# Kernel tuning notes

Hardware: AMD Instinct MI355X
Metric: run time of the kernel (lower is better)

## Reference

```python
import jax, jax.numpy as jnp
import numpy as np

TAU = 2.0
V_TH = 1.0
ALPHA = 2.0  # ATan surrogate alpha

@jax.custom_vjp
def spike_fn(x):
    return (x >= 0.0).astype(x.dtype)

def _spike_fwd(x):
    return spike_fn(x), x

def _spike_bwd(x, g):
    # spikingjelly ATan surrogate: alpha/2 / (1 + (pi/2*alpha*x)^2)
    return (g * (ALPHA / 2.0) / (1.0 + (jnp.pi / 2.0 * ALPHA * x) ** 2),)

spike_fn.defvjp(_spike_fwd, _spike_bwd)

def lif_step(v, h):
    # decay_input=True, v_reset=0: v += (h - v)/tau
    v = v + (h - v) / TAU
    s = spike_fn(v - V_TH)
    v = v * (1.0 - s)  # hard reset to v_reset=0
    return v, s

def setup_inputs() -> dict:
    key = jax.random.key(0)
    k1, k2, k3 = jax.random.split(key, 3)
    B, T, I, H, O = 128, 2048, 128, 1024, 128
    x = jax.random.normal(k1, (B, T, I), dtype=jnp.float32)
    W1 = jax.random.normal(k2, (H, I), dtype=jnp.float32) / np.sqrt(I)
    b1 = jnp.zeros((H,), dtype=jnp.float32)
    W2 = jax.random.normal(k3, (O, H), dtype=jnp.float32) / np.sqrt(H)
    b2 = jnp.zeros((O,), dtype=jnp.float32)
    return {"x": x, "W1": W1, "b1": b1, "W2": W2, "b2": b2}

def reference(x, W1, b1, W2, b2):
    B, T, I = x.shape
    H = W1.shape[0]
    O = W2.shape[0]
    xt = jnp.transpose(x, (1, 0, 2))  # [T, B, I]

    def step(carry, x_t):
        v1, v2 = carry
        h1 = x_t @ W1.T + b1
        v1, s1 = lif_step(v1, h1)
        h2 = s1 @ W2.T + b2
        v2, s2 = lif_step(v2, h2)
        return (v1, v2), s2

    v1_0 = jnp.zeros((B, H), dtype=x.dtype)
    v2_0 = jnp.zeros((B, O), dtype=x.dtype)
    _, outs = jax.lax.scan(step, (v1_0, v2_0), xt)  # [T, B, O]
    decision_start = T // 2
    return jnp.sum(outs[decision_start:], axis=0)  # [B, O]
```

## Files before the change

kernel.cpp:

```cpp
#include <hip/hip_runtime.h>
#include <stdint.h>

#define NB 128
#define NT 2048
#define NI 128
#define NH 1024
#define NO 128

typedef float f32x4 __attribute__((ext_vector_type(4)));
typedef float f32x16 __attribute__((ext_vector_type(16)));

__global__ __launch_bounds__(256) void w2p_kernel(
    const float* __restrict__ W2, float2* __restrict__ W2P)
{
    const int idx = blockIdx.x * 256 + threadIdx.x;
    const int k = idx >> 6;
    const int j = idx & 63;
    W2P[idx] = make_float2(W2[(size_t)j * NH + k], W2[(size_t)(j + 64) * NH + k]);
}

#define XL(DST, IMM)                                                      \
    asm volatile("s_load_dwordx16 %0, %1, " #IMM : "=s"(DST) : "s"(xb))

#define F16(ACC, XV)                                                      \
    do {                                                                  \
        ACC = fmaf(w0.x, (XV)[0],  ACC);                                  \
        ACC = fmaf(w0.y, (XV)[1],  ACC);                                  \
        ACC = fmaf(w0.z, (XV)[2],  ACC);                                  \
        ACC = fmaf(w0.w, (XV)[3],  ACC);                                  \
        ACC = fmaf(w1.x, (XV)[4],  ACC);                                  \
        ACC = fmaf(w1.y, (XV)[5],  ACC);                                  \
        ACC = fmaf(w1.z, (XV)[6],  ACC);                                  \
        ACC = fmaf(w1.w, (XV)[7],  ACC);                                  \
        ACC = fmaf(w2.x, (XV)[8],  ACC);                                  \
        ACC = fmaf(w2.y, (XV)[9],  ACC);                                  \
        ACC = fmaf(w2.z, (XV)[10], ACC);                                  \
        ACC = fmaf(w2.w, (XV)[11], ACC);                                  \
        ACC = fmaf(w3.x, (XV)[12], ACC);                                  \
        ACC = fmaf(w3.y, (XV)[13], ACC);                                  \
        ACC = fmaf(w3.z, (XV)[14], ACC);                                  \
        ACC = fmaf(w3.w, (XV)[15], ACC);                                  \
    } while (0)

#define KCHUNK(Q0, I0, I1, I2, I3)                                        \
    {                                                                     \
        f32x16 xv0, xv1, xv2, xv3;                                        \
        XL(xv0, I0); XL(xv1, I1); XL(xv2, I2); XL(xv3, I3);               \
        asm volatile("s_waitcnt lgkmcnt(0)"                               \
                     : "+s"(xv0), "+s"(xv1), "+s"(xv2), "+s"(xv3));       \
        const f32x4 w0 = wrow[(Q0) + 0];                                  \
        const f32x4 w1 = wrow[(Q0) + 1];                                  \
        const f32x4 w2 = wrow[(Q0) + 2];                                  \
        const f32x4 w3 = wrow[(Q0) + 3];                                  \
        F16(t0, xv0); F16(t1, xv1); F16(t2, xv2); F16(t3, xv3);           \
    }

#define LIFSTEP(TT, TACC)                                                 \
    {                                                                     \
        const float h1 = ((TACC + red[par][0][TT][lane]) +                \
                          (red[par][1][TT][lane] + red[par][2][TT][lane])) + \
                         bias;                                            \
        v = fmaf(h1 - v, 0.5f, v);                                        \
        const bool sp = (v >= 1.0f);                                      \
        v = sp ? 0.0f : v;                                                \
        const unsigned long long m = __ballot(sp);                        \
        if (lane == 0) s1w[(size_t)TT * NB * (NH / 64)] = (uint64_t)m;    \
    }

__global__ __launch_bounds__(256, 4) void snn_phaseA4(
    const float* __restrict__ x, const float* __restrict__ W1,
    const float* __restrict__ b1, uint64_t* __restrict__ s1bits)
{
    const int b = blockIdx.x >> 4;
    const int hg = blockIdx.x & 15;
    const int kq = __builtin_amdgcn_readfirstlane(threadIdx.x >> 6);
    const int lane = threadIdx.x & 63;
    const int h = hg * 64 + lane;

    __shared__ f32x4 wlds[64][33];
    __shared__ float red[2][3][4][64];

#pragma unroll
    for (int i = 0; i < 8; ++i) {
        const int c = threadIdx.x + i * 256;
        const int r = c >> 5;
        const int kc = c & 31;
        wlds[r][kc] = *reinterpret_cast<const f32x4*>(
            W1 + (size_t)(hg * 64 + r) * NI + kc * 4);
    }
    __syncthreads();

    const float bias = b1[h];
    const f32x4* __restrict__ wrow = &wlds[lane][0];
    const int wb = kq * 8;

    const float* xb = x + (size_t)b * NT * NI + kq * 32;
    uint64_t* s1w = s1bits + (size_t)b * (NH / 64) + hg;

    float v = 0.0f;
#pragma unroll 1
    for (int tc = 0; tc < NT; tc += 4) {
        float t0 = 0.f, t1 = 0.f, t2 = 0.f, t3 = 0.f;
        KCHUNK(wb + 0, 0x0,  0x200, 0x400, 0x600);
        KCHUNK(wb + 4, 0x40, 0x240, 0x440, 0x640);

        const int par = (tc >> 2) & 1;
        if (kq) {
            red[par][kq - 1][0][lane] = t0;
            red[par][kq - 1][1][lane] = t1;
            red[par][kq - 1][2][lane] = t2;
            red[par][kq - 1][3][lane] = t3;
        }
        __syncthreads();
        if (!kq) {
            LIFSTEP(0, t0);
            LIFSTEP(1, t1);
            LIFSTEP(2, t2);
            LIFSTEP(3, t3);
        }
        s1w += (size_t)4 * NB * (NH / 64);
        xb += 4 * NI;
    }
}

__global__ __launch_bounds__(256, 4) void snn_phaseB(
    const uint64_t* __restrict__ s1bits, const float2* __restrict__ W2P,
    float* __restrict__ h2)
{
    const int wv = threadIdx.x >> 6;
    const int lane = threadIdx.x & 63;
    const size_t m = (size_t)blockIdx.x * 4 + wv;

    const uint64_t* __restrict__ sb = s1bits + m * (NH / 64);
    float a0 = 0.f, a1 = 0.f;

#pragma unroll 1
    for (int wd = 0; wd < NH / 64; ++wd) {
        const uint64_t m64 = sb[wd];
        const uint32_t mlo = (uint32_t)__builtin_amdgcn_readfirstlane((int)(uint32_t)m64);
        const uint32_t mhi = (uint32_t)__builtin_amdgcn_readfirstlane((int)(uint32_t)(m64 >> 32));
        uint64_t msk = ((uint64_t)mhi << 32) | mlo;
        while (msk) {
            const int i = __builtin_ctzll(msk);
            msk &= (msk - 1);
            const size_t k = ((size_t)wd << 6) + i;
            const float2 ww = W2P[k * 64 + lane];
            a0 += ww.x;
            a1 += ww.y;
        }
    }
    h2[m * NO + lane] = a0;
    h2[m * NO + 64 + lane] = a1;
}

__global__ __launch_bounds__(64) void snn_phaseD(
    const float* __restrict__ h2, const float* __restrict__ b2,
    float* __restrict__ out)
{
    const int idx = blockIdx.x * 64 + threadIdx.x;
    const int b = idx >> 7;
    const int o = idx & 127;
    const float bias = b2[o];

    const float* __restrict__ p = h2 + (size_t)b * NO + o;
    float v = 0.f, c = 0.f;
#pragma unroll 16
    for (int t = 0; t < NT; ++t) {
        const float hh = p[(size_t)t * NB * NO] + bias;
        v = fmaf(hh - v, 0.5f, v);
        const bool s = (v >= 1.0f);
        v = s ? 0.f : v;
        if (t >= NT / 2) c += s ? 1.f : 0.f;
    }
    out[idx] = c;
}

extern "C" void kernel_launch(void* const* d_in, const int* in_sizes, int n_in,
                              void* d_out, int out_size, void* d_ws,
                              size_t ws_size, hipStream_t stream)
{
    const float* x  = (const float*)d_in[0];
    const float* W1 = (const float*)d_in[1];
    const float* b1 = (const float*)d_in[2];
    const float* W2 = (const float*)d_in[3];
    const float* b2 = (const float*)d_in[4];
    float* out = (float*)d_out;

    uint8_t* ws = (uint8_t*)d_ws;
    uint64_t* s1bits = (uint64_t*)ws;
    float2* W2P = (float2*)(ws + (size_t)NT * NB * (NH / 64) * 8);
    float* h2 = (float*)(ws + (size_t)NT * NB * (NH / 64) * 8 +
                         (size_t)NH * 64 * sizeof(float2));

    w2p_kernel<<<dim3((NH * 64) / 256), dim3(256), 0, stream>>>(W2, W2P);
    snn_phaseA4<<<dim3(NB * 16), dim3(256), 0, stream>>>(x, W1, b1, s1bits);
    snn_phaseB<<<dim3((NT * NB) / 4), dim3(256), 0, stream>>>(s1bits, W2P, h2);
    snn_phaseD<<<dim3(256), dim3(64), 0, stream>>>(h2, b2, out);
}
```

Baseline: 2.319 ms.

## Prefetch x tiles into LDS with async global_load_lds double buffering

Replaces the per-wave scalar s_load_dwordx16 fetches of x, which stalled on lgkmcnt(0) every chunk, with direct global-to-LDS async loads. Each step loads the next 4 timesteps of x into a double-buffered LDS tile while the current one is computed, and the FMAs read x from LDS as vectors. Occupancy hint drops from 4 to 3 blocks. This adds LDS traffic, a vmcnt wait before each barrier and lower occupancy in exchange for overlapping the x loads with compute.

```diff
diff --git a/kernel.cpp b/kernel.cpp
--- a/kernel.cpp
+++ b/kernel.cpp
@@ -8,7 +8,6 @@
 #define NO 128
 
 typedef float f32x4 __attribute__((ext_vector_type(4)));
-typedef float f32x16 __attribute__((ext_vector_type(16)));
 
 __global__ __launch_bounds__(256) void w2p_kernel(
     const float* __restrict__ W2, float2* __restrict__ W2P)
@@ -18,42 +17,6 @@
     const int j = idx & 63;
     W2P[idx] = make_float2(W2[(size_t)j * NH + k], W2[(size_t)(j + 64) * NH + k]);
 }
-
-#define XL(DST, IMM)                                                      \
-    asm volatile("s_load_dwordx16 %0, %1, " #IMM : "=s"(DST) : "s"(xb))
-
-#define F16(ACC, XV)                                                      \
-    do {                                                                  \
-        ACC = fmaf(w0.x, (XV)[0],  ACC);                                  \
-        ACC = fmaf(w0.y, (XV)[1],  ACC);                                  \
-        ACC = fmaf(w0.z, (XV)[2],  ACC);                                  \
-        ACC = fmaf(w0.w, (XV)[3],  ACC);                                  \
-        ACC = fmaf(w1.x, (XV)[4],  ACC);                                  \
-        ACC = fmaf(w1.y, (XV)[5],  ACC);                                  \
-        ACC = fmaf(w1.z, (XV)[6],  ACC);                                  \
-        ACC = fmaf(w1.w, (XV)[7],  ACC);                                  \
-        ACC = fmaf(w2.x, (XV)[8],  ACC);                                  \
-        ACC = fmaf(w2.y, (XV)[9],  ACC);                                  \
-        ACC = fmaf(w2.z, (XV)[10], ACC);                                  \
-        ACC = fmaf(w2.w, (XV)[11], ACC);                                  \
-        ACC = fmaf(w3.x, (XV)[12], ACC);                                  \
-        ACC = fmaf(w3.y, (XV)[13], ACC);                                  \
-        ACC = fmaf(w3.z, (XV)[14], ACC);                                  \
-        ACC = fmaf(w3.w, (XV)[15], ACC);                                  \
-    } while (0)
-
-#define KCHUNK(Q0, I0, I1, I2, I3)                                        \
-    {                                                                     \
-        f32x16 xv0, xv1, xv2, xv3;                                        \
-        XL(xv0, I0); XL(xv1, I1); XL(xv2, I2); XL(xv3, I3);               \
-        asm volatile("s_waitcnt lgkmcnt(0)"                               \
-                     : "+s"(xv0), "+s"(xv1), "+s"(xv2), "+s"(xv3));       \
-        const f32x4 w0 = wrow[(Q0) + 0];                                  \
-        const f32x4 w1 = wrow[(Q0) + 1];                                  \
-        const f32x4 w2 = wrow[(Q0) + 2];                                  \
-        const f32x4 w3 = wrow[(Q0) + 3];                                  \
-        F16(t0, xv0); F16(t1, xv1); F16(t2, xv2); F16(t3, xv3);           \
-    }
 
 #define LIFSTEP(TT, TACC)                                                 \
     {                                                                     \
@@ -67,18 +30,20 @@
         if (lane == 0) s1w[(size_t)TT * NB * (NH / 64)] = (uint64_t)m;    \
     }
 
-__global__ __launch_bounds__(256, 4) void snn_phaseA4(
+__global__ __launch_bounds__(256, 3) void snn_phaseA5(
     const float* __restrict__ x, const float* __restrict__ W1,
     const float* __restrict__ b1, uint64_t* __restrict__ s1bits)
 {
     const int b = blockIdx.x >> 4;
     const int hg = blockIdx.x & 15;
-    const int kq = __builtin_amdgcn_readfirstlane(threadIdx.x >> 6);
+    const int wv = threadIdx.x >> 6;
+    const int kq = __builtin_amdgcn_readfirstlane(wv);
     const int lane = threadIdx.x & 63;
     const int h = hg * 64 + lane;
 
     __shared__ f32x4 wlds[64][33];
     __shared__ float red[2][3][4][64];
+    __shared__ float xlds[2][4][128];
 
 #pragma unroll
     for (int i = 0; i < 8; ++i) {
@@ -88,29 +53,74 @@
         wlds[r][kc] = *reinterpret_cast<const f32x4*>(
             W1 + (size_t)(hg * 64 + r) * NI + kc * 4);
     }
+
+    const float* __restrict__ xrow = x + (size_t)b * NT * NI;
+    if (wv < 2) {
+        __builtin_amdgcn_global_load_lds(xrow + wv * 256 + lane * 4,
+                                         &xlds[0][wv * 2][0], 16, 0, 0);
+    }
+    asm volatile("s_waitcnt vmcnt(0)" ::: "memory");
     __syncthreads();
 
     const float bias = b1[h];
     const f32x4* __restrict__ wrow = &wlds[lane][0];
     const int wb = kq * 8;
 
-    const float* xb = x + (size_t)b * NT * NI + kq * 32;
     uint64_t* s1w = s1bits + (size_t)b * (NH / 64) + hg;
 
     float v = 0.0f;
 #pragma unroll 1
     for (int tc = 0; tc < NT; tc += 4) {
+        const int par = (tc >> 2) & 1;
+        if (wv < 2 && tc + 4 < NT) {
+            __builtin_amdgcn_global_load_lds(
+                xrow + (size_t)(tc + 4) * NI + wv * 256 + lane * 4,
+                &xlds[par ^ 1][wv * 2][0], 16, 0, 0);
+        }
+
         float t0 = 0.f, t1 = 0.f, t2 = 0.f, t3 = 0.f;
-        KCHUNK(wb + 0, 0x0,  0x200, 0x400, 0x600);
-        KCHUNK(wb + 4, 0x40, 0x240, 0x440, 0x640);
-
-        const int par = (tc >> 2) & 1;
+#pragma unroll
+        for (int half = 0; half < 2; ++half) {
+            const f32x4 w0 = wrow[wb + half * 4 + 0];
+            const f32x4 w1 = wrow[wb + half * 4 + 1];
+            const f32x4 w2 = wrow[wb + half * 4 + 2];
+            const f32x4 w3 = wrow[wb + half * 4 + 3];
+            const float* xk = &xlds[par][0][kq * 32 + half * 16];
+#pragma unroll
+            for (int tt = 0; tt < 4; ++tt) {
+                const f32x4 xq0 = *reinterpret_cast<const f32x4*>(xk + tt * 128 + 0);
+                const f32x4 xq1 = *reinterpret_cast<const f32x4*>(xk + tt * 128 + 4);
+                const f32x4 xq2 = *reinterpret_cast<const f32x4*>(xk + tt * 128 + 8);
+                const f32x4 xq3 = *reinterpret_cast<const f32x4*>(xk + tt * 128 + 12);
+                float acc = (tt == 0) ? t0 : (tt == 1) ? t1 : (tt == 2) ? t2 : t3;
+                acc = fmaf(w0.x, xq0[0], acc);
+                acc = fmaf(w0.y, xq0[1], acc);
+                acc = fmaf(w0.z, xq0[2], acc);
+                acc = fmaf(w0.w, xq0[3], acc);
+                acc = fmaf(w1.x, xq1[0], acc);
+                acc = fmaf(w1.y, xq1[1], acc);
+                acc = fmaf(w1.z, xq1[2], acc);
+                acc = fmaf(w1.w, xq1[3], acc);
+                acc = fmaf(w2.x, xq2[0], acc);
+                acc = fmaf(w2.y, xq2[1], acc);
+                acc = fmaf(w2.z, xq2[2], acc);
+                acc = fmaf(w2.w, xq2[3], acc);
+                acc = fmaf(w3.x, xq3[0], acc);
+                acc = fmaf(w3.y, xq3[1], acc);
+                acc = fmaf(w3.z, xq3[2], acc);
+                acc = fmaf(w3.w, xq3[3], acc);
+                if (tt == 0) t0 = acc; else if (tt == 1) t1 = acc;
+                else if (tt == 2) t2 = acc; else t3 = acc;
+            }
+        }
+
         if (kq) {
             red[par][kq - 1][0][lane] = t0;
             red[par][kq - 1][1][lane] = t1;
             red[par][kq - 1][2][lane] = t2;
             red[par][kq - 1][3][lane] = t3;
         }
+        asm volatile("s_waitcnt vmcnt(0)" ::: "memory");
         __syncthreads();
         if (!kq) {
             LIFSTEP(0, t0);
@@ -119,7 +129,6 @@
             LIFSTEP(3, t3);
         }
         s1w += (size_t)4 * NB * (NH / 64);
-        xb += 4 * NI;
     }
 }
 
@@ -193,7 +202,7 @@
                          (size_t)NH * 64 * sizeof(float2));
 
     w2p_kernel<<<dim3((NH * 64) / 256), dim3(256), 0, stream>>>(W2, W2P);
-    snn_phaseA4<<<dim3(NB * 16), dim3(256), 0, stream>>>(x, W1, b1, s1bits);
+    snn_phaseA5<<<dim3(NB * 16), dim3(256), 0, stream>>>(x, W1, b1, s1bits);
     snn_phaseB<<<dim3((NT * NB) / 4), dim3(256), 0, stream>>>(s1bits, W2P, h2);
     snn_phaseD<<<dim3(256), dim3(64), 0, stream>>>(h2, b2, out);
 }
```

After: 2.551 ms. 1.1x slower.

## Split phase A K-reduction across eight waves per block instead of four

Applied to the files above, without the earlier changes.

Phase A now launches 512-thread blocks with eight waves, each handling a 16-wide K slice instead of 32, and reduces seven partials through a larger LDS buffer. Wave-to-slice assignment is rotated by block index so that co-resident blocks, and with them the scalar x loads and LDS weight reads, are staggered. The aim is to shorten the serial per-timestep dependency chain and add more latency hiding. The cost is more LDS traffic and more additions in the reduction step, heavier barrier synchronisation across eight waves, and higher LDS use per block.

```diff
diff --git a/kernel.cpp b/kernel.cpp
--- a/kernel.cpp
+++ b/kernel.cpp
@@ -42,24 +42,14 @@
         ACC = fmaf(w3.w, (XV)[15], ACC);                                  \
     } while (0)
 
-#define KCHUNK(Q0, I0, I1, I2, I3)                                        \
-    {                                                                     \
-        f32x16 xv0, xv1, xv2, xv3;                                        \
-        XL(xv0, I0); XL(xv1, I1); XL(xv2, I2); XL(xv3, I3);               \
-        asm volatile("s_waitcnt lgkmcnt(0)"                               \
-                     : "+s"(xv0), "+s"(xv1), "+s"(xv2), "+s"(xv3));       \
-        const f32x4 w0 = wrow[(Q0) + 0];                                  \
-        const f32x4 w1 = wrow[(Q0) + 1];                                  \
-        const f32x4 w2 = wrow[(Q0) + 2];                                  \
-        const f32x4 w3 = wrow[(Q0) + 3];                                  \
-        F16(t0, xv0); F16(t1, xv1); F16(t2, xv2); F16(t3, xv3);           \
-    }
-
 #define LIFSTEP(TT, TACC)                                                 \
     {                                                                     \
-        const float h1 = ((TACC + red[par][0][TT][lane]) +                \
-                          (red[par][1][TT][lane] + red[par][2][TT][lane])) + \
-                         bias;                                            \
+        const float h1 =                                                  \
+            (((TACC + red[par][0][TT][lane]) +                            \
+              (red[par][1][TT][lane] + red[par][2][TT][lane])) +          \
+             ((red[par][3][TT][lane] + red[par][4][TT][lane]) +           \
+              (red[par][5][TT][lane] + red[par][6][TT][lane]))) +         \
+            bias;                                                         \
         v = fmaf(h1 - v, 0.5f, v);                                        \
         const bool sp = (v >= 1.0f);                                      \
         v = sp ? 0.0f : v;                                                \
@@ -67,22 +57,23 @@
         if (lane == 0) s1w[(size_t)TT * NB * (NH / 64)] = (uint64_t)m;    \
     }
 
-__global__ __launch_bounds__(256, 4) void snn_phaseA4(
+__global__ __launch_bounds__(512, 6) void snn_phaseA6(
     const float* __restrict__ x, const float* __restrict__ W1,
     const float* __restrict__ b1, uint64_t* __restrict__ s1bits)
 {
     const int b = blockIdx.x >> 4;
     const int hg = blockIdx.x & 15;
-    const int kq = __builtin_amdgcn_readfirstlane(threadIdx.x >> 6);
+    const int wv = threadIdx.x >> 6;
+    const int kq = __builtin_amdgcn_readfirstlane((wv + blockIdx.x) & 7);
     const int lane = threadIdx.x & 63;
     const int h = hg * 64 + lane;
 
     __shared__ f32x4 wlds[64][33];
-    __shared__ float red[2][3][4][64];
+    __shared__ float red[2][7][4][64];
 
 #pragma unroll
-    for (int i = 0; i < 8; ++i) {
-        const int c = threadIdx.x + i * 256;
+    for (int i = 0; i < 4; ++i) {
+        const int c = threadIdx.x + i * 512;
         const int r = c >> 5;
         const int kc = c & 31;
         wlds[r][kc] = *reinterpret_cast<const f32x4*>(
@@ -92,17 +83,33 @@
 
     const float bias = b1[h];
     const f32x4* __restrict__ wrow = &wlds[lane][0];
-    const int wb = kq * 8;
-
-    const float* xb = x + (size_t)b * NT * NI + kq * 32;
+    const int wb = kq * 4;
+
+    const float* xb = x + (size_t)b * NT * NI + kq * 16;
     uint64_t* s1w = s1bits + (size_t)b * (NH / 64) + hg;
 
     float v = 0.0f;
 #pragma unroll 1
     for (int tc = 0; tc < NT; tc += 4) {
+        f32x16 xv0, xv1, xv2, xv3;
+        XL(xv0, 0x0);
+        XL(xv1, 0x200);
+        XL(xv2, 0x400);
+        XL(xv3, 0x600);
+        asm volatile("s_waitcnt lgkmcnt(0)"
+                     : "+s"(xv0), "+s"(xv1), "+s"(xv2), "+s"(xv3));
+        __builtin_amdgcn_sched_barrier(0);
+
+        const f32x4 w0 = wrow[wb + 0];
+        const f32x4 w1 = wrow[wb + 1];
+        const f32x4 w2 = wrow[wb + 2];
+        const f32x4 w3 = wrow[wb + 3];
+
         float t0 = 0.f, t1 = 0.f, t2 = 0.f, t3 = 0.f;
-        KCHUNK(wb + 0, 0x0,  0x200, 0x400, 0x600);
-        KCHUNK(wb + 4, 0x40, 0x240, 0x440, 0x640);
+        F16(t0, xv0);
+        F16(t1, xv1);
+        F16(t2, xv2);
+        F16(t3, xv3);
 
         const int par = (tc >> 2) & 1;
         if (kq) {
@@ -193,7 +200,7 @@
                          (size_t)NH * 64 * sizeof(float2));
 
     w2p_kernel<<<dim3((NH * 64) / 256), dim3(256), 0, stream>>>(W2, W2P);
-    snn_phaseA4<<<dim3(NB * 16), dim3(256), 0, stream>>>(x, W1, b1, s1bits);
+    snn_phaseA6<<<dim3(NB * 16), dim3(512), 0, stream>>>(x, W1, b1, s1bits);
     snn_phaseB<<<dim3((NT * NB) / 4), dim3(256), 0, stream>>>(s1bits, W2P, h2);
     snn_phaseD<<<dim3(256), dim3(64), 0, stream>>>(h2, b2, out);
 }
```

Measured after the change: 2.082 ms. 1.11x faster.
